# Optimization experiments

Measured on AMD Instinct MI355X. Metric: run time of the kernel, lower is better.

Reference implementation:

```python
import jax, jax.numpy as jnp
import numpy as np

RESID = 1024
HEADS = 16
HEAD_DIM = 64


def setup_inputs() -> dict:
    key = jax.random.key(0)
    ks = jax.random.split(key, 6)
    B, S = 2, 2048
    residual_stream = jax.random.normal(ks[0], (B, S, RESID), dtype=jnp.float32)
    # per-head qkv linear params, stacked over heads: [H, resid, 3*head_dim]
    W_qkv = jax.random.normal(ks[1], (HEADS, RESID, 3 * HEAD_DIM), dtype=jnp.float32) * (1.0 / np.sqrt(RESID))
    b_qkv = jax.random.normal(ks[2], (HEADS, 3 * HEAD_DIM), dtype=jnp.float32) * 0.01
    # output projection resid -> resid
    W_o = jax.random.normal(ks[3], (RESID, RESID), dtype=jnp.float32) * (1.0 / np.sqrt(RESID))
    b_o = jax.random.normal(ks[4], (RESID,), dtype=jnp.float32) * 0.01
    return {"residual_stream": residual_stream, "W_qkv": W_qkv, "b_qkv": b_qkv, "W_o": W_o, "b_o": b_o}


def reference(residual_stream, W_qkv, b_qkv, W_o, b_o):
    # qkv per head: [B, H, S, 3*D]
    qkv = jnp.einsum('bsr,hrd->bhsd', residual_stream, W_qkv) + b_qkv[None, :, None, :]
    q = qkv[..., :HEAD_DIM]
    k = qkv[..., HEAD_DIM:2 * HEAD_DIM]
    v = qkv[..., 2 * HEAD_DIM:]
    # NOTE: original has no causal mask; softmax over full key axis
    scores = jnp.einsum('bhsd,bhtd->bhst', q, k) / jnp.sqrt(jnp.float32(HEAD_DIM))
    attn = jax.nn.softmax(scores, axis=-1)
    out = jnp.einsum('bhst,bhtd->bhsd', attn, v)  # [B, H, S, D]
    B, H, S, D = out.shape
    out = out.transpose(0, 2, 1, 3).reshape(B, S, H * D)  # concat heads -> [B, S, resid]
    return out @ W_o + b_o
```

## Files before the change

### kernel.cpp

```cpp
#include <hip/hip_runtime.h>
#include <hip/hip_bf16.h>

#define B_ 2
#define S_ 2048
#define H_ 16
#define HD 64
#define R_ 1024
#define N_ (B_*S_)

typedef unsigned short ushort_t;
typedef short bf16x8 __attribute__((ext_vector_type(8)));
typedef float f32x4 __attribute__((ext_vector_type(4)));
typedef float f32x16 __attribute__((ext_vector_type(16)));

#define MFMA(a,b,c) __builtin_amdgcn_mfma_f32_16x16x32_bf16(a,b,c,0,0,0)
#define MFMA32(a,b,c) __builtin_amdgcn_mfma_f32_32x32x16_bf16(a,b,c,0,0,0)
#define GLD16(g,l) __builtin_amdgcn_global_load_lds( \
    (const __attribute__((address_space(1))) void*)(g), \
    (__attribute__((address_space(3))) void*)(l), 16, 0, 0)

__device__ __forceinline__ unsigned short f2bf(float f) {
  unsigned int u = __builtin_bit_cast(unsigned int, f);
  u += 0x7fffu + ((u >> 16) & 1u);
  return (unsigned short)(u >> 16);
}

__device__ __forceinline__ unsigned int cvtpk(float lo, float hi) {
  unsigned int r;
  asm("v_cvt_pk_bf16_f32 %0, %1, %2" : "=v"(r) : "v"(lo), "v"(hi));
  return r;
}

__device__ __forceinline__ void plswap(unsigned int &a, unsigned int &b) {
  asm volatile("v_permlane32_swap_b32 %0, %1" : "+v"(a), "+v"(b));
}

#if __has_builtin(__builtin_amdgcn_exp2f)
__device__ __forceinline__ float EXP2(float x) { return __builtin_amdgcn_exp2f(x); }
#else
__device__ __forceinline__ float EXP2(float x) {
  float r; asm("v_exp_f32 %0, %1" : "=v"(r) : "v"(x)); return r;
}
#endif

#if __has_builtin(__builtin_amdgcn_rcpf)
__device__ __forceinline__ float RCP(float x) { return __builtin_amdgcn_rcpf(x); }
#else
__device__ __forceinline__ float RCP(float x) { return 1.0f / x; }
#endif

__device__ __forceinline__ bf16x8 ld8(const ushort_t* p) {
  return *(const bf16x8*)p;
}

__device__ __forceinline__ void transpose_tile(const float* __restrict__ in,
                                               ushort_t* __restrict__ out,
                                               int rows, int cols, int rt, int ct,
                                               float (*t)[65], int tid) {
  const int r0 = rt * 64, c0 = ct * 64;
  const int tx = tid & 63, ty = tid >> 6;
  #pragma unroll
  for (int i = 0; i < 16; i++) {
    int r = ty * 16 + i;
    t[r][tx] = in[(size_t)(r0 + r) * cols + c0 + tx];
  }
  __syncthreads();
  #pragma unroll
  for (int i = 0; i < 16; i++) {
    int c = ty * 16 + i;
    out[(size_t)(c0 + c) * rows + r0 + tx] = f2bf(t[tx][c]);
  }
}

__global__ __launch_bounds__(256) void k_prep(
    const float* __restrict__ x, ushort_t* __restrict__ xb,
    const float* __restrict__ Wqkv, ushort_t* __restrict__ WT,
    const float* __restrict__ Wo, ushort_t* __restrict__ WoT) {
  __shared__ float t[64][65];
  const int bid = blockIdx.x, tid = threadIdx.x;
  if (bid < 4096) {
    int i = bid * 256 + tid;
    float4 v = ((const float4*)x)[i];
    ushort4 o;
    o.x = f2bf(v.x); o.y = f2bf(v.y); o.z = f2bf(v.z); o.w = f2bf(v.w);
    ((ushort4*)xb)[i] = o;
  } else if (bid < 4096 + 768) {
    int tt = bid - 4096;
    int z = tt / 48, rem = tt % 48;
    transpose_tile(Wqkv + (size_t)z * 1024 * 192, WT + (size_t)z * 192 * 1024,
                   1024, 192, rem % 16, rem / 16, t, tid);
  } else {
    int tt = bid - (4096 + 768);
    transpose_tile(Wo, WoT, 1024, 1024, tt % 16, tt / 16, t, tid);
  }
}

__global__ __launch_bounds__(256, 3) void k_qkv(
    const ushort_t* __restrict__ Xb, const ushort_t* __restrict__ WT,
    const float* __restrict__ bqkv,
    ushort_t* __restrict__ Q, ushort_t* __restrict__ K, ushort_t* __restrict__ Vt) {
  __shared__ ushort_t lA[2][128 * 32];
  __shared__ ushort_t lB[2][128 * 32];
  const int m0 = blockIdx.x * 128;
  const int n0 = blockIdx.y * 128;
  const int tid = threadIdx.x;
  const int w = tid >> 6, l = tid & 63;
  const int lr = l & 15, lg = l >> 4;
  const int wr = w >> 1, wc = w & 1;

  const ushort_t* Asrc = Xb + (size_t)m0 * R_;
  const ushort_t* Bsrc = WT + (size_t)n0 * R_;
  const int arow = l >> 2;
  const int acol = ((l & 3) ^ ((arow >> 1) & 3)) * 8;

  f32x4 acc[4][4];
  const f32x4 fz = {0.f, 0.f, 0.f, 0.f};
  #pragma unroll
  for (int m = 0; m < 4; m++)
    #pragma unroll
    for (int n = 0; n < 4; n++) acc[m][n] = fz;

  auto stage = [&](int buf, int kt) {
    const int k0 = kt * 32;
    #pragma unroll
    for (int i = 0; i < 2; i++) {
      int chunk = w + 4 * i;
      GLD16(Asrc + (size_t)(chunk * 16 + arow) * R_ + k0 + acol, &lA[buf][chunk * 512]);
      GLD16(Bsrc + (size_t)(chunk * 16 + arow) * R_ + k0 + acol, &lB[buf][chunk * 512]);
    }
  };

  stage(0, 0);
  asm volatile("s_waitcnt vmcnt(0)" ::: "memory");
  __syncthreads();

  const int rsw = (lr >> 1) & 3;
  int cur = 0;
  for (int kt = 0; kt < 32; ++kt) {
    if (kt < 31) stage(cur ^ 1, kt + 1);
    bf16x8 af[4], bfr[4];
    #pragma unroll
    for (int m = 0; m < 4; m++)
      af[m] = ld8(&lA[cur][(wr * 64 + m * 16 + lr) * 32 + ((lg ^ rsw) * 8)]);
    #pragma unroll
    for (int n = 0; n < 4; n++)
      bfr[n] = ld8(&lB[cur][(wc * 64 + n * 16 + lr) * 32 + ((lg ^ rsw) * 8)]);
    __builtin_amdgcn_s_setprio(1);
    #pragma unroll
    for (int m = 0; m < 4; m++)
      #pragma unroll
      for (int n = 0; n < 4; n++)
        acc[m][n] = MFMA(af[m], bfr[n], acc[m][n]);
    __builtin_amdgcn_s_setprio(0);
    asm volatile("s_waitcnt vmcnt(0)" ::: "memory");
    __syncthreads();
    cur ^= 1;
  }

  #pragma unroll
  for (int n = 0; n < 4; n++) {
    const int col = n0 + wc * 64 + n * 16 + lr;
    const int h = col / 192;
    const int cc = col - h * 192;
    const float bias = bqkv[col];
    #pragma unroll
    for (int m = 0; m < 4; m++) {
      const int rb = m0 + wr * 64 + m * 16 + lg * 4;
      #pragma unroll
      for (int r = 0; r < 4; r++) {
        float v = acc[m][n][r] + bias;
        int srow = rb + r;
        int b = srow >> 11, s = srow & 2047;
        size_t bh = (size_t)b * H_ + h;
        if (cc < 64) {
          Q[(bh * S_ + s) * HD + cc] = f2bf(v * 0.1803368801111137f);
        } else if (cc < 128) {
          int d = cc - 64;
          K[(bh * S_ + s) * HD + d] = f2bf(v);
        } else {
          int d = cc - 128;
          Vt[(bh * HD + d) * S_ + s] = f2bf(v);
        }
      }
    }
  }
}

__global__ __launch_bounds__(256, 2) void k_attn(
    const ushort_t* __restrict__ Q, const ushort_t* __restrict__ K,
    const ushort_t* __restrict__ Vt, ushort_t* __restrict__ AO) {
  __shared__ ushort_t sK[3][64 * 64];
  __shared__ ushort_t sV[3][64 * 64];
  const int qt = blockIdx.x;
  const int bh = blockIdx.y;
  const int b = bh >> 4, h = bh & 15;
  const int tid = threadIdx.x, w = tid >> 6, l = tid & 63;
  const int lq = l & 31, hi = l >> 5;

  const ushort_t* Qb = Q + (size_t)bh * S_ * HD;
  const ushort_t* Kb = K + (size_t)bh * S_ * HD;
  const ushort_t* Vb = Vt + (size_t)bh * HD * S_;

  bf16x8 qf[4];
  {
    int qrow = qt * 128 + 32 * w + lq;
    #pragma unroll
    for (int kd = 0; kd < 4; kd++)
      qf[kd] = ld8(&Qb[(size_t)qrow * HD + kd * 16 + hi * 8]);
  }

  const int sr = l >> 3;
  const int scol = l & 7;
  const int r0l = w * 16 + sr;
  const ushort_t* kp = Kb + (size_t)r0l * HD + scol * 8;
  const ushort_t* vp = Vb + (size_t)r0l * S_ + scol * 8;
  bf16x8 kreg0, kreg1, vreg0, vreg1;
  int tnext = 0;
  auto issue = [&]() {
    if (tnext < 32) {
      kreg0 = ld8(kp); kreg1 = ld8(kp + 8 * HD);
      vreg0 = ld8(vp); vreg1 = ld8(vp + 8 * S_);
      kp += 64 * HD; vp += 64;
    }
    ++tnext;
  };
  const int coff0 = r0l * 64 + ((scol ^ sr) * 8);
  const int coff1 = coff0 + 8 * 64;
  auto commit = [&](ushort_t* bK, ushort_t* bV) {
    *(bf16x8*)&bK[coff0] = kreg0; *(bf16x8*)&bK[coff1] = kreg1;
    *(bf16x8*)&bV[coff0] = vreg0; *(bf16x8*)&bV[coff1] = vreg1;
  };

  const f32x16 fz16 = {0};
  const bf16x8 onesv = {0x3F80, 0x3F80, 0x3F80, 0x3F80, 0x3F80, 0x3F80, 0x3F80, 0x3F80};
  f32x16 oacc0 = fz16, oacc1 = fz16, ssv = fz16;

  const int c = hi ^ (lq & 7);

  auto QK = [&](const ushort_t* bK, f32x16& s0, f32x16& s1) {
    f32x16 a0 = fz16, a1 = fz16;
    __builtin_amdgcn_s_setprio(1);
    #pragma unroll
    for (int kd = 0; kd < 4; kd++) {
      const int sl = ((kd * 2) ^ c) * 8;
      bf16x8 ka0 = ld8(&bK[lq * 64 + sl]);
      bf16x8 ka1 = ld8(&bK[(32 + lq) * 64 + sl]);
      a0 = MFMA32(ka0, qf[kd], a0);
      a1 = MFMA32(ka1, qf[kd], a1);
    }
    __builtin_amdgcn_s_setprio(0);
    s0 = a0; s1 = a1;
  };

  auto SMPV = [&](const ushort_t* bV, f32x16 s0, f32x16 s1) {
    #pragma unroll
    for (int n = 0; n < 2; n++) {
      const f32x16 scv = n ? s1 : s0;
      float e[16];
      #pragma unroll
      for (int r = 0; r < 16; r++) e[r] = EXP2(scv[r]);
      #pragma unroll
      for (int sl2 = 0; sl2 < 2; sl2++) {
        unsigned int X  = cvtpk(e[8 * sl2 + 0], e[8 * sl2 + 1]);
        unsigned int Y  = cvtpk(e[8 * sl2 + 2], e[8 * sl2 + 3]);
        unsigned int X2 = cvtpk(e[8 * sl2 + 4], e[8 * sl2 + 5]);
        unsigned int Y2 = cvtpk(e[8 * sl2 + 6], e[8 * sl2 + 7]);
        plswap(X, X2);
        plswap(Y, Y2);
        int4 wv = {(int)X, (int)Y, (int)X2, (int)Y2};
        bf16x8 pa = __builtin_bit_cast(bf16x8, wv);
        const int ks = n * 2 + sl2;
        const int sl3 = ((ks * 2) ^ c) * 8;
        __builtin_amdgcn_s_setprio(1);
        ssv = MFMA32(pa, onesv, ssv);
        {
          bf16x8 vb0 = ld8(&bV[lq * 64 + sl3]);
          bf16x8 vb1 = ld8(&bV[(32 + lq) * 64 + sl3]);
          oacc0 = MFMA32(pa, vb0, oacc0);
          oacc1 = MFMA32(pa, vb1, oacc1);
        }
        __builtin_amdgcn_s_setprio(0);
      }
    }
  };

  f32x16 scA0, scA1, scB0, scB1;
  issue();
  commit(sK[0], sV[0]);
  issue();
  __syncthreads();
  QK(sK[0], scA0, scA1);
  commit(sK[1], sV[1]);
  __syncthreads();
  issue();

#define ABODY(C, N, O, SI0, SI1, SO0, SO1) \
    QK(sK[N], SO0, SO1); \
    SMPV(sV[C], SI0, SI1); \
    commit(sK[O], sV[O]); \
    issue(); \
    __syncthreads();

  for (int kt = 0; kt < 30; kt += 6) {
    ABODY(0, 1, 2, scA0, scA1, scB0, scB1)
    ABODY(1, 2, 0, scB0, scB1, scA0, scA1)
    ABODY(2, 0, 1, scA0, scA1, scB0, scB1)
    ABODY(0, 1, 2, scB0, scB1, scA0, scA1)
    ABODY(1, 2, 0, scA0, scA1, scB0, scB1)
    ABODY(2, 0, 1, scB0, scB1, scA0, scA1)
  }
#undef ABODY

  QK(sK[1], scB0, scB1);
  SMPV(sV[0], scA0, scA1);
  SMPV(sV[1], scB0, scB1);

  #pragma unroll
  for (int reg = 0; reg < 16; reg++) {
    float inv = RCP(ssv[reg]);
    int qloc = (reg & 3) + 8 * (reg >> 2) + 4 * hi;
    int s = qt * 128 + 32 * w + qloc;
    AO[(size_t)(b * S_ + s) * R_ + h * HD + lq] = f2bf(oacc0[reg] * inv);
    AO[(size_t)(b * S_ + s) * R_ + h * HD + 32 + lq] = f2bf(oacc1[reg] * inv);
  }
}

__global__ __launch_bounds__(256, 2) void k_out(
    const ushort_t* __restrict__ AO, const ushort_t* __restrict__ WoT,
    const float* __restrict__ bo, float* __restrict__ out) {
  __shared__ ushort_t lA[2][128 * 32];
  __shared__ ushort_t lB[2][128 * 32];
  const int m0 = blockIdx.x * 128, n0 = blockIdx.y * 128;
  const int tid = threadIdx.x, w = tid >> 6, l = tid & 63;
  const int lr = l & 15, lg = l >> 4;
  const int wr = w >> 1, wc = w & 1;
  const ushort_t* Asrc = AO + (size_t)m0 * R_;
  const ushort_t* Bsrc = WoT + (size_t)n0 * R_;
  const int arow = l >> 2;
  const int acol = ((l & 3) ^ ((arow >> 1) & 3)) * 8;

  f32x4 acc[4][4];
  const f32x4 fz = {0.f, 0.f, 0.f, 0.f};
  #pragma unroll
  for (int m = 0; m < 4; m++)
    #pragma unroll
    for (int n = 0; n < 4; n++) acc[m][n] = fz;

  auto stage = [&](int buf, int kt) {
    const int k0 = kt * 32;
    #pragma unroll
    for (int i = 0; i < 2; i++) {
      int chunk = w + 4 * i;
      GLD16(Asrc + (size_t)(chunk * 16 + arow) * R_ + k0 + acol, &lA[buf][chunk * 512]);
      GLD16(Bsrc + (size_t)(chunk * 16 + arow) * R_ + k0 + acol, &lB[buf][chunk * 512]);
    }
  };

  stage(0, 0);
  asm volatile("s_waitcnt vmcnt(0)" ::: "memory");
  __syncthreads();

  const int rsw = (lr >> 1) & 3;
  int cur = 0;
  for (int kt = 0; kt < 32; ++kt) {
    if (kt < 31) stage(cur ^ 1, kt + 1);
    bf16x8 af[4], bfr[4];
    #pragma unroll
    for (int m = 0; m < 4; m++)
      af[m] = ld8(&lA[cur][(wr * 64 + m * 16 + lr) * 32 + ((lg ^ rsw) * 8)]);
    #pragma unroll
    for (int n = 0; n < 4; n++)
      bfr[n] = ld8(&lB[cur][(wc * 64 + n * 16 + lr) * 32 + ((lg ^ rsw) * 8)]);
    __builtin_amdgcn_s_setprio(1);
    #pragma unroll
    for (int m = 0; m < 4; m++)
      #pragma unroll
      for (int n = 0; n < 4; n++)
        acc[m][n] = MFMA(af[m], bfr[n], acc[m][n]);
    __builtin_amdgcn_s_setprio(0);
    asm volatile("s_waitcnt vmcnt(0)" ::: "memory");
    __syncthreads();
    cur ^= 1;
  }

  #pragma unroll
  for (int n = 0; n < 4; n++) {
    const int col = n0 + wc * 64 + n * 16 + lr;
    const float bias = bo[col];
    #pragma unroll
    for (int m = 0; m < 4; m++) {
      const int row = m0 + wr * 64 + m * 16 + lg * 4;
      #pragma unroll
      for (int r = 0; r < 4; r++)
        out[(size_t)(row + r) * R_ + col] = acc[m][n][r] + bias;
    }
  }
}

extern "C" void kernel_launch(void* const* d_in, const int* in_sizes, int n_in,
                              void* d_out, int out_size, void* d_ws, size_t ws_size,
                              hipStream_t stream) {
  const float* resid = (const float*)d_in[0];
  const float* Wqkv  = (const float*)d_in[1];
  const float* bqkv  = (const float*)d_in[2];
  const float* Wo    = (const float*)d_in[3];
  const float* bo    = (const float*)d_in[4];
  float* out = (float*)d_out;

  ushort_t* Xb  = (ushort_t*)d_ws;
  ushort_t* WT  = Xb  + (size_t)N_ * R_;
  ushort_t* WoT = WT  + (size_t)H_ * 192 * R_;
  ushort_t* Qd  = WoT + (size_t)R_ * R_;
  ushort_t* Kd  = Qd  + (size_t)B_ * H_ * S_ * HD;
  ushort_t* Vtd = Kd  + (size_t)B_ * H_ * S_ * HD;
  ushort_t* AOd = Vtd + (size_t)B_ * H_ * S_ * HD;

  k_prep<<<dim3(4096 + 768 + 256), dim3(256), 0, stream>>>(resid, Xb, Wqkv, WT, Wo, WoT);
  k_qkv<<<dim3(32, 24), dim3(256), 0, stream>>>(Xb, WT, bqkv, Qd, Kd, Vtd);
  k_attn<<<dim3(16, 32), dim3(256), 0, stream>>>(Qd, Kd, Vtd, AOd);
  k_out<<<dim3(32, 8), dim3(256), 0, stream>>>(AOd, WoT, bo, out);
}
```

Baseline: 117.7 us.

## Deepen GEMM prefetch pipelines and relax barriers in attention kernel

The QKV GEMM moves from double to triple buffering and the output GEMM to quadruple buffering. Each now keeps two or three K-tiles of global→LDS loads in flight, using partial vmcnt waits instead of draining all loads every iteration. The attention kernel's __syncthreads calls become barriers that wait only on LDS/scalar counters, so outstanding global loads are no longer forced to complete at each barrier. The aim is to hide memory latency behind MFMA work, at the cost of more LDS per block. The fixed vmcnt thresholds may not wait for the last tiles in the final iterations, which risks a race unless the compiler adds its own waits.

```diff
diff --git a/kernel.cpp b/kernel.cpp
--- a/kernel.cpp
+++ b/kernel.cpp
@@ -18,6 +18,13 @@
 #define GLD16(g,l) __builtin_amdgcn_global_load_lds( \
     (const __attribute__((address_space(1))) void*)(g), \
     (__attribute__((address_space(3))) void*)(l), 16, 0, 0)
+
+#define WAITBAR(N) do { \
+    asm volatile("s_waitcnt vmcnt(" #N ")" ::: "memory"); \
+    __builtin_amdgcn_s_barrier(); } while (0)
+#define DSBAR() do { \
+    asm volatile("s_waitcnt lgkmcnt(0)" ::: "memory"); \
+    __builtin_amdgcn_s_barrier(); } while (0)
 
 __device__ __forceinline__ unsigned short f2bf(float f) {
   unsigned int u = __builtin_bit_cast(unsigned int, f);
@@ -99,8 +106,8 @@
     const ushort_t* __restrict__ Xb, const ushort_t* __restrict__ WT,
     const float* __restrict__ bqkv,
     ushort_t* __restrict__ Q, ushort_t* __restrict__ K, ushort_t* __restrict__ Vt) {
-  __shared__ ushort_t lA[2][128 * 32];
-  __shared__ ushort_t lB[2][128 * 32];
+  __shared__ ushort_t lA[3][128 * 32];
+  __shared__ ushort_t lB[3][128 * 32];
   const int m0 = blockIdx.x * 128;
   const int n0 = blockIdx.y * 128;
   const int tid = threadIdx.x;
@@ -131,13 +138,13 @@
   };
 
   stage(0, 0);
-  asm volatile("s_waitcnt vmcnt(0)" ::: "memory");
-  __syncthreads();
+  stage(1, 1);
 
   const int rsw = (lr >> 1) & 3;
-  int cur = 0;
+  int cur = 0, nxt = 2;
   for (int kt = 0; kt < 32; ++kt) {
-    if (kt < 31) stage(cur ^ 1, kt + 1);
+    WAITBAR(4);
+    if (kt + 2 < 32) stage(nxt, kt + 2);
     bf16x8 af[4], bfr[4];
     #pragma unroll
     for (int m = 0; m < 4; m++)
@@ -152,9 +159,8 @@
       for (int n = 0; n < 4; n++)
         acc[m][n] = MFMA(af[m], bfr[n], acc[m][n]);
     __builtin_amdgcn_s_setprio(0);
-    asm volatile("s_waitcnt vmcnt(0)" ::: "memory");
-    __syncthreads();
-    cur ^= 1;
+    cur = (cur == 2) ? 0 : cur + 1;
+    nxt = (nxt == 2) ? 0 : nxt + 1;
   }
 
   #pragma unroll
@@ -288,10 +294,10 @@
   issue();
   commit(sK[0], sV[0]);
   issue();
-  __syncthreads();
+  DSBAR();
   QK(sK[0], scA0, scA1);
   commit(sK[1], sV[1]);
-  __syncthreads();
+  DSBAR();
   issue();
 
 #define ABODY(C, N, O, SI0, SI1, SO0, SO1) \
@@ -299,7 +305,7 @@
     SMPV(sV[C], SI0, SI1); \
     commit(sK[O], sV[O]); \
     issue(); \
-    __syncthreads();
+    DSBAR();
 
   for (int kt = 0; kt < 30; kt += 6) {
     ABODY(0, 1, 2, scA0, scA1, scB0, scB1)
@@ -328,8 +334,8 @@
 __global__ __launch_bounds__(256, 2) void k_out(
     const ushort_t* __restrict__ AO, const ushort_t* __restrict__ WoT,
     const float* __restrict__ bo, float* __restrict__ out) {
-  __shared__ ushort_t lA[2][128 * 32];
-  __shared__ ushort_t lB[2][128 * 32];
+  __shared__ ushort_t lA[4][128 * 32];
+  __shared__ ushort_t lB[4][128 * 32];
   const int m0 = blockIdx.x * 128, n0 = blockIdx.y * 128;
   const int tid = threadIdx.x, w = tid >> 6, l = tid & 63;
   const int lr = l & 15, lg = l >> 4;
@@ -357,13 +363,14 @@
   };
 
   stage(0, 0);
-  asm volatile("s_waitcnt vmcnt(0)" ::: "memory");
-  __syncthreads();
+  stage(1, 1);
+  stage(2, 2);
 
   const int rsw = (lr >> 1) & 3;
-  int cur = 0;
+  int cur = 0, nxt = 3;
   for (int kt = 0; kt < 32; ++kt) {
-    if (kt < 31) stage(cur ^ 1, kt + 1);
+    WAITBAR(8);
+    if (kt + 3 < 32) stage(nxt, kt + 3);
     bf16x8 af[4], bfr[4];
     #pragma unroll
     for (int m = 0; m < 4; m++)
@@ -378,9 +385,8 @@
       for (int n = 0; n < 4; n++)
         acc[m][n] = MFMA(af[m], bfr[n], acc[m][n]);
     __builtin_amdgcn_s_setprio(0);
-    asm volatile("s_waitcnt vmcnt(0)" ::: "memory");
-    __syncthreads();
-    cur ^= 1;
+    cur = (cur + 1) & 3;
+    nxt = (nxt + 1) & 3;
   }
 
   #pragma unroll
```

Result: no change. 117.1 us, median of 2 (-0.5%).
